# Performance work log

Measured on AMD Instinct MI355X. Metric: run time of the kernel, lower is better.

The kernel has to match this reference:

```python
import jax, jax.numpy as jnp
from jax import lax
import numpy as np

B = 256
# conv stack: (in_ch, out_ch, kernel)
_CONV_CFG = [(1, 3, 4), (3, 9, 4), (9, 12, 4), (12, 15, 4), (15, 15, 3)]
_FLAT = 15 * 4 ** 4  # 3840, matches nn.Linear(15*(18-14)**4, 100)


def _conv4d(x, w, b):
    """True 4D valid convolution. x: [B,C,d1,d2,d3,d4], w: [O,I,k,k,k,k]."""
    dn = lax.conv_dimension_numbers(x.shape, w.shape, ('NCDHWX', 'OIDHWX', 'NCDHWX'))
    y = lax.conv_general_dilated(x, w, window_strides=(1, 1, 1, 1),
                                 padding='VALID', dimension_numbers=dn)
    return y + b.reshape((1, -1) + (1,) * 4)


def setup_inputs() -> dict:
    key = jax.random.key(0)
    ks = jax.random.split(key, 16)
    inp = {'x': jax.random.normal(ks[0], (B, 1, 18, 18, 18, 18), dtype=jnp.float32)}
    for i, (ci, co, k) in enumerate(_CONV_CFG, start=1):
        fan_in = ci * k ** 4
        inp[f'w{i}'] = jax.random.normal(ks[2 * i - 1], (co, ci, k, k, k, k), dtype=jnp.float32) / np.sqrt(fan_in)
        inp[f'b{i}'] = jnp.zeros((co,), dtype=jnp.float32)
    inp['fc1_w'] = jax.random.normal(ks[11], (_FLAT, 100), dtype=jnp.float32) / np.sqrt(_FLAT)
    inp['fc1_b'] = jnp.zeros((100,), dtype=jnp.float32)
    inp['fc2_w'] = jax.random.normal(ks[12], (100, 1), dtype=jnp.float32) / np.sqrt(100.0)
    inp['fc2_b'] = jnp.zeros((1,), dtype=jnp.float32)
    return inp


def reference(x, w1, b1, w2, b2, w3, b3, w4, b4, w5, b5, fc1_w, fc1_b, fc2_w, fc2_b):
    h = jax.nn.relu(_conv4d(x, w1, b1))
    h = jax.nn.relu(_conv4d(h, w2, b2))
    h = jax.nn.relu(_conv4d(h, w3, b3))
    h = jax.nn.relu(_conv4d(h, w4, b4))
    h = jax.nn.relu(_conv4d(h, w5, b5))  # [B,15,4,4,4,4]
    h = h.reshape(h.shape[0], -1)        # [B,3840], torch Flatten order
    # Dropout(0.5) is identity at inference (eval mode)
    h = jax.nn.relu(h @ fc1_w + fc1_b)
    return jax.nn.sigmoid(h @ fc2_w + fc2_b)  # [B,1]
```

## Files before the change

kernel.cpp:

```cpp
#include <hip/hip_runtime.h>
#include <hip/hip_bf16.h>


#define BATCH 256
typedef unsigned int u32;
typedef float    f32x4  __attribute__((ext_vector_type(4)));
typedef float    f32x16 __attribute__((ext_vector_type(16)));
typedef _Float16 f16x8  __attribute__((ext_vector_type(8)));

struct __attribute__((packed, aligned(4))) f16x8w { f16x8 v; };

__global__ void cvt_f32_f16(const float* __restrict__ in, _Float16* __restrict__ o, int n8) {
    int i = blockIdx.x * blockDim.x + threadIdx.x;
    if (i >= n8) return;
    const f32x4* p = (const f32x4*)(in + (size_t)i * 8);
    f32x4 a = p[0], b = p[1];
    f16x8 v;
    #pragma unroll
    for (int j = 0; j < 4; ++j) { v[j] = (_Float16)a[j]; v[4 + j] = (_Float16)b[j]; }
    *(f16x8*)(o + (size_t)i * 8) = v;
}

template<int COUT, int CIN, int KS, int S>
__global__ void prepack_v5(const float* __restrict__ w, _Float16* __restrict__ wf) {
    constexpr int STEPS = CIN * KS * 2 * KS;
    constexpr int TOT = STEPS * 512;
    int idx = blockIdx.x * 256 + threadIdx.x;
    if (idx >= TOT) return;
    int j    = idx & 7;
    int lane = (idx >> 3) & 63;
    int st   = idx >> 9;
    int k1 = st % KS;
    int r1 = st / KS;
    int k3p = r1 & 1;
    int r2  = r1 >> 1;
    int k2 = r2 % KS;
    int ci = r2 / KS;
    int gg = lane >> 5, col = lane & 31;
    int oc = col / S, s = col % S;
    int k3 = k3p * 2 + gg;
    int k4 = j - s;
    float v = 0.0f;
    if (oc < COUT && k3 < KS && k4 >= 0 && k4 < KS)
        v = w[((((oc * CIN + ci) * KS + k1) * KS + k2) * KS + k3) * KS + k4];
    wf[idx] = (_Float16)v;
}

template<int BYTES>
__device__ __forceinline__ void stage_b(const _Float16* gsrc, char* ldst, int tid) {
    constexpr int N16 = BYTES / 16;
    const int wv = tid >> 6, ln = tid & 63;
    #pragma unroll
    for (int it = 0; it * 256 < N16; ++it) {
        int u16 = it * 256 + (wv << 6);
        if (u16 < N16) {
            const char* gp = (const char*)gsrc + (size_t)(u16 + ln) * 16;
            __builtin_amdgcn_global_load_lds(
                (const __attribute__((address_space(1))) unsigned int*)gp,
                (__attribute__((address_space(3))) unsigned int*)(ldst + u16 * 16),
                16, 0, 0);
        }
    }
}

template<int CIN, int COUT, int KS, int DIN, int DP, int S, int OP, int T,
         int CG, int MINW>
__launch_bounds__(256, MINW)
__global__ void conv4d_v10(const _Float16* __restrict__ x,
                           const _Float16* __restrict__ wf,
                           const float* __restrict__ bias,
                           _Float16* __restrict__ out) {
    constexpr int DOUT = DIN - KS + 1;
    constexpr int NB   = (DOUT + S - 1) / S;
    constexpr int PCOL = DOUT * DOUT * NB;
    constexpr int NTC  = (PCOL + 31) / 32;
    constexpr int NG   = DOUT / T;
    static_assert(DOUT % T == 0, "T must divide DOUT");
    constexpr int XD2 = DIN * DP;
    constexpr int XD1 = DIN * XD2;
    constexpr int XCI = DIN * XD1;
    constexpr int GROUPS = CIN * KS * 2;
    static_assert(GROUPS % CG == 0, "CG must divide GROUPS");
    constexpr int CSTEPS = CG * KS;
    constexpr int CBYTES = CSTEPS * 1024;
    constexpr int NCHUNK = GROUPS / CG;
    constexpr int NBUF   = (NCHUNK > 1) ? 2 : 1;
    constexpr int AJ = T + KS - 1;
    constexpr int W  = T + 1;
    constexpr u32 NW   = (u32)BATCH * NG * NTC;
    constexpr u32 POUT = (u32)DOUT * DOUT * DOUT * OP;

    __shared__ char bsm[NBUF * CBYTES];
    const int tid = threadIdx.x;
    u32 wid = blockIdx.x * 4u + (u32)(tid >> 6);
    if (wid >= NW) wid = NW - 1u;
    const int ln = tid & 63;
    const int g  = ln >> 5;
    const int r  = ln & 31;

    u32 tc = wid % (u32)NTC;  u32 q = wid / (u32)NTC;
    u32 d1g = q % (u32)NG;    u32 b = q / (u32)NG;
    u32 rr = tc * 32u + (u32)r;  if (rr >= (u32)PCOL) rr = (u32)PCOL - 1u;
    u32 u  = rr % (u32)NB;    u32 q2 = rr / (u32)NB;
    u32 d3 = q2 % (u32)DOUT;  u32 d2 = q2 / (u32)DOUT;

    const u32 lanebase2 = (b * (u32)(CIN * XCI) + d1g * (u32)(T * XD1)
                         + d2 * (u32)XD2 + d3 * (u32)DP + (u32)(g * DP)
                         + u * (u32)S) * 2u;
    const char* xc = (const char*)x;

    f32x16 acc[T];
    #pragma unroll
    for (int t = 0; t < T; ++t)
        #pragma unroll
        for (int i = 0; i < 16; ++i) acc[t][i] = 0.0f;

    stage_b<CBYTES>(wf, &bsm[0], tid);

    #pragma unroll 1
    for (int ch = 0; ch < NCHUNK; ++ch) {
        __syncthreads();
        if (NCHUNK > 1 && ch + 1 < NCHUNK)
            stage_b<CBYTES>(wf + (size_t)(ch + 1) * CSTEPS * 512,
                            &bsm[((ch + 1) & 1) * CBYTES], tid);
        const char* bb = &bsm[(ch & 1) * (NBUF > 1 ? CBYTES : 0)] + ln * 16;
        #pragma unroll
        for (int gi = 0; gi < CG; ++gi) {
            int grp = ch * CG + gi;
            int k3p = grp & 1;
            int k2  = (grp >> 1) % KS;
            int ci  = (grp >> 1) / KS;
            u32 goff = ((u32)ci * (u32)XCI + (u32)k2 * (u32)XD2
                      + (u32)(k3p * 2 * DP)) * 2u;
            const char* ap = xc + lanebase2 + goff;

            f16x8 ar[W];
            #pragma unroll
            for (int j = 0; j < T; ++j)
                ar[j] = ((const f16x8w*)(ap + j * (XD1 * 2)))->v;
            #pragma unroll
            for (int k1 = 0; k1 < KS; ++k1) {
                if (T + k1 < AJ)
                    ar[(T + k1) % W] = ((const f16x8w*)(ap + (T + k1) * (XD1 * 2)))->v;
                f16x8 bf = *(const f16x8*)(bb + (gi * KS + k1) * 1024);
                #pragma unroll
                for (int t = 0; t < T; ++t)
                    acc[t] = __builtin_amdgcn_mfma_f32_32x32x16_f16(
                        ar[(k1 + t) % W], bf, acc[t], 0, 0, 0);
            }
        }
    }

    const int oc = r / S, s = r % S;
    if (oc >= COUT) return;
    float bv = bias[oc];
    #pragma unroll
    for (int reg = 0; reg < 16; ++reg) {
        int rowoff = (reg & 3) + 8 * (reg >> 2) + 4 * g;
        u32 rr2 = tc * 32u + (u32)rowoff;
        if (rr2 >= (u32)PCOL) rr2 = (u32)PCOL - 1u;
        u32 uu = rr2 % (u32)NB;  u32 qq = rr2 / (u32)NB;
        u32 dd3 = qq % (u32)DOUT; u32 dd2 = qq / (u32)DOUT;
        u32 d4 = uu * (u32)S + (u32)s;
        if (d4 < (u32)DOUT) {
            u32 obase = (b * (u32)COUT + (u32)oc) * POUT
                      + (dd2 * (u32)DOUT + dd3) * (u32)OP + d4
                      + d1g * (u32)(T * DOUT * DOUT * OP);
            #pragma unroll
            for (int t = 0; t < T; ++t)
                out[obase + (u32)t * (u32)(DOUT * DOUT * OP)]
                    = (_Float16)fmaxf(acc[t][reg] + bv, 0.0f);
        }
    }
}

__global__ void prepack_fc1(const float* __restrict__ w, _Float16* __restrict__ wf) {
    int idx = blockIdx.x * 256 + threadIdx.x;
    if (idx >= 430080) return;
    int j    = idx & 7;
    int lane = (idx >> 3) & 63;
    int t9   = idx >> 9;
    int st   = t9 % 120;
    int ni   = t9 / 120;
    int k    = st * 32 + (lane >> 4) * 8 + j;
    int col  = ni * 16 + (lane & 15);
    wf[idx] = (_Float16)((col < 100) ? w[k * 100 + col] : 0.0f);
}

__launch_bounds__(256)
__global__ void fc1_mfma(const _Float16* __restrict__ h,
                         const _Float16* __restrict__ wfc,
                         const float* __restrict__ bias,
                         float* __restrict__ o) {
    int wv   = blockIdx.x * 4 + (threadIdx.x >> 6);
    int lane = threadIdx.x & 63;
    int r = lane & 15, g = lane >> 4;
    int mi = wv / 7, ni = wv % 7;
    const f16x8* A  = (const f16x8*)(h + (size_t)(mi * 16 + r) * 3840);
    const f16x8* Bv = (const f16x8*)wfc;
    f32x4 acc = {0.f, 0.f, 0.f, 0.f};
    #pragma unroll 4
    for (int st = 0; st < 120; ++st) {
        f16x8 a = A[st * 4 + g];
        f16x8 b = Bv[(ni * 120 + st) * 64 + lane];
        acc = __builtin_amdgcn_mfma_f32_16x16x32_f16(a, b, acc, 0, 0, 0);
    }
    int col = ni * 16 + r;
    if (col < 100) {
        float bv = bias[col];
        #pragma unroll
        for (int i = 0; i < 4; ++i) {
            int row = mi * 16 + g * 4 + i;
            o[row * 100 + col] = fmaxf(acc[i] + bv, 0.0f);
        }
    }
}

__global__ void fc2_sigmoid(const float* __restrict__ h,
                            const float* __restrict__ w,
                            const float* __restrict__ bias,
                            float* __restrict__ out) {
    int b = blockIdx.x * blockDim.x + threadIdx.x;
    if (b >= BATCH) return;
    const float* hb = h + b * 100;
    float acc = bias[0];
    #pragma unroll
    for (int j = 0; j < 100; ++j)
        acc = fmaf(hb[j], w[j], acc);
    out[b] = 1.0f / (1.0f + expf(-acc));
}

extern "C" void kernel_launch(void* const* d_in, const int* in_sizes, int n_in,
                              void* d_out, int out_size, void* d_ws, size_t ws_size,
                              hipStream_t stream) {
    const float* x    = (const float*)d_in[0];
    const float* w1   = (const float*)d_in[1];
    const float* b1   = (const float*)d_in[2];
    const float* w2   = (const float*)d_in[3];
    const float* b2   = (const float*)d_in[4];
    const float* w3   = (const float*)d_in[5];
    const float* b3   = (const float*)d_in[6];
    const float* w4   = (const float*)d_in[7];
    const float* b4   = (const float*)d_in[8];
    const float* w5   = (const float*)d_in[9];
    const float* b5   = (const float*)d_in[10];
    const float* fc1w = (const float*)d_in[11];
    const float* fc1b = (const float*)d_in[12];
    const float* fc2w = (const float*)d_in[13];
    const float* fc2b = (const float*)d_in[14];
    float* out = (float*)d_out;

    _Float16* W = (_Float16*)d_ws;
    size_t cur = 0;
    auto alloc = [&](size_t n) { _Float16* p = W + cur; cur += (n + 255) & ~(size_t)255; return p; };
    _Float16* x16 = alloc(26873856);
    _Float16* h1  = alloc(41472000);
    _Float16* h2  = alloc(47775744);
    _Float16* h3  = alloc(22394880);
    _Float16* h4  = alloc(4976640);
    _Float16* h5  = alloc(983040);
    _Float16* wf1 = alloc(16384);
    _Float16* wf2 = alloc(49152);
    _Float16* wf3 = alloc(147456);
    _Float16* wf4 = alloc(196608);
    _Float16* wf5 = alloc(138240);
    _Float16* wfc = alloc(430080);
    float* fc1out = (float*)alloc(51200 + 256);

    cvt_f32_f16<<<13122, 256, 0, stream>>>(x, x16, 3359232);

    prepack_v5<3, 1, 4, 4><<<64,  256, 0, stream>>>(w1, wf1);
    prepack_v5<9, 3, 4, 2><<<192, 256, 0, stream>>>(w2, wf2);
    prepack_v5<12, 9, 4, 2><<<576, 256, 0, stream>>>(w3, wf3);
    prepack_v5<15, 12, 4, 2><<<768, 256, 0, stream>>>(w4, wf4);
    prepack_v5<15, 15, 3, 2><<<540, 256, 0, stream>>>(w5, wf5);
    prepack_fc1<<<1680, 256, 0, stream>>>(fc1w, wfc);

    conv4d_v10<1, 3, 4, 18, 18, 4, 16, 3, 8, 4><<<9280, 256, 0, stream>>>(x16, wf1, b1, h1);
    conv4d_v10<3, 9, 4, 15, 16, 2, 12, 6, 4, 3><<<3456, 256, 0, stream>>>(h1, wf2, b2, h2);
    conv4d_v10<9, 12, 4, 12, 12, 2, 10, 3, 4, 4><<<2496, 256, 0, stream>>>(h2, wf3, b3, h3);
    conv4d_v10<12, 15, 4, 9, 10, 2, 6, 3, 4, 4><<<512, 256, 0, stream>>>(h3, wf4, b4, h4);
    conv4d_v10<15, 15, 3, 6, 6, 2, 4, 4, 6, 4><<<64, 256, 0, stream>>>(h4, wf5, b5, h5);

    fc1_mfma<<<28, 256, 0, stream>>>(h5, wfc, fc1b, fc1out);
    fc2_sigmoid<<<1, 256, 0, stream>>>(fc1out, fc2w, fc2b, out);
}
```

Baseline: 931.3 us.

## Write shifted copy of conv1 output so conv2 uses stride-3 column packing

Conv1 now also writes a copy of its output shifted by one element. Conv2 reads from this copy whenever its base offset is odd, so its 16-byte A-fragment loads stay aligned even with a stride S of 3. Conv2 moves from stride 2 to stride 3 packing, which reduces its column tiles and launch size (2304 blocks instead of 3456). Its weights are prepacked for S=3 and workspace buffers are reused to fit the extra copy. The cost is roughly double the store traffic for conv1's large output.

```diff
diff --git a/kernel.cpp b/kernel.cpp
--- a/kernel.cpp
+++ b/kernel.cpp
@@ -64,12 +64,14 @@
 }
 
 template<int CIN, int COUT, int KS, int DIN, int DP, int S, int OP, int T,
-         int CG, int MINW>
+         int CG, int MINW, int SODD, int WSHIFT>
 __launch_bounds__(256, MINW)
-__global__ void conv4d_v10(const _Float16* __restrict__ x,
+__global__ void conv4d_v13(const _Float16* __restrict__ x,
+                           const _Float16* __restrict__ xs,
                            const _Float16* __restrict__ wf,
                            const float* __restrict__ bias,
-                           _Float16* __restrict__ out) {
+                           _Float16* __restrict__ out,
+                           _Float16* __restrict__ outs) {
     constexpr int DOUT = DIN - KS + 1;
     constexpr int NB   = (DOUT + S - 1) / S;
     constexpr int PCOL = DOUT * DOUT * NB;
@@ -104,10 +106,16 @@
     u32 u  = rr % (u32)NB;    u32 q2 = rr / (u32)NB;
     u32 d3 = q2 % (u32)DOUT;  u32 d2 = q2 / (u32)DOUT;
 
-    const u32 lanebase2 = (b * (u32)(CIN * XCI) + d1g * (u32)(T * XD1)
-                         + d2 * (u32)XD2 + d3 * (u32)DP + (u32)(g * DP)
-                         + u * (u32)S) * 2u;
-    const char* xc = (const char*)x;
+    const u32 o = b * (u32)(CIN * XCI) + d1g * (u32)(T * XD1)
+                + d2 * (u32)XD2 + d3 * (u32)DP + (u32)(g * DP) + u * (u32)S;
+    const char* xb;
+    if (SODD) {
+        u32 p = o & 1u;
+        xb = p ? ((const char*)xs + (size_t)(o - 1u) * 2)
+               : ((const char*)x  + (size_t)o * 2);
+    } else {
+        xb = (const char*)x + (size_t)o * 2;
+    }
 
     f32x16 acc[T];
     #pragma unroll
@@ -132,7 +140,7 @@
             int ci  = (grp >> 1) / KS;
             u32 goff = ((u32)ci * (u32)XCI + (u32)k2 * (u32)XD2
                       + (u32)(k3p * 2 * DP)) * 2u;
-            const char* ap = xc + lanebase2 + goff;
+            const char* ap = xb + goff;
 
             f16x8 ar[W];
             #pragma unroll
@@ -167,9 +175,12 @@
                       + (dd2 * (u32)DOUT + dd3) * (u32)OP + d4
                       + d1g * (u32)(T * DOUT * DOUT * OP);
             #pragma unroll
-            for (int t = 0; t < T; ++t)
-                out[obase + (u32)t * (u32)(DOUT * DOUT * OP)]
-                    = (_Float16)fmaxf(acc[t][reg] + bv, 0.0f);
+            for (int t = 0; t < T; ++t) {
+                u32 oidx = obase + (u32)t * (u32)(DOUT * DOUT * OP);
+                _Float16 v = (_Float16)fmaxf(acc[t][reg] + bv, 0.0f);
+                out[oidx] = v;
+                if (WSHIFT) { if (oidx >= 1u) outs[oidx - 1u] = v; }
+            }
         }
     }
 }
@@ -251,36 +262,40 @@
     float* out = (float*)d_out;
 
     _Float16* W = (_Float16*)d_ws;
-    size_t cur = 0;
-    auto alloc = [&](size_t n) { _Float16* p = W + cur; cur += (n + 255) & ~(size_t)255; return p; };
-    _Float16* x16 = alloc(26873856);
-    _Float16* h1  = alloc(41472000);
-    _Float16* h2  = alloc(47775744);
-    _Float16* h3  = alloc(22394880);
-    _Float16* h4  = alloc(4976640);
-    _Float16* h5  = alloc(983040);
-    _Float16* wf1 = alloc(16384);
-    _Float16* wf2 = alloc(49152);
-    _Float16* wf3 = alloc(147456);
-    _Float16* wf4 = alloc(196608);
-    _Float16* wf5 = alloc(138240);
-    _Float16* wfc = alloc(430080);
-    float* fc1out = (float*)alloc(51200 + 256);
+    _Float16* x16 = W;
+    _Float16* h1  = W + 26873856;
+    _Float16* h1s = W + 68345856;
+    _Float16* h2  = W + 109817856;
+    _Float16* wf1 = W + 157593600;
+    _Float16* wf2 = W + 157609984;
+    _Float16* wf3 = W + 157659136;
+    _Float16* wf4 = W + 157806592;
+    _Float16* wf5 = W + 158003200;
+    _Float16* wfc = W + 158141440;
+    float* fc1out = (float*)(W + 158571520);
+    _Float16* h3  = h1s;
+    _Float16* h4  = h1s + 22394880;
+    _Float16* h5  = h1s + 27371520;
 
     cvt_f32_f16<<<13122, 256, 0, stream>>>(x, x16, 3359232);
 
     prepack_v5<3, 1, 4, 4><<<64,  256, 0, stream>>>(w1, wf1);
-    prepack_v5<9, 3, 4, 2><<<192, 256, 0, stream>>>(w2, wf2);
+    prepack_v5<9, 3, 4, 3><<<192, 256, 0, stream>>>(w2, wf2);
     prepack_v5<12, 9, 4, 2><<<576, 256, 0, stream>>>(w3, wf3);
     prepack_v5<15, 12, 4, 2><<<768, 256, 0, stream>>>(w4, wf4);
     prepack_v5<15, 15, 3, 2><<<540, 256, 0, stream>>>(w5, wf5);
     prepack_fc1<<<1680, 256, 0, stream>>>(fc1w, wfc);
 
-    conv4d_v10<1, 3, 4, 18, 18, 4, 16, 3, 8, 4><<<9280, 256, 0, stream>>>(x16, wf1, b1, h1);
-    conv4d_v10<3, 9, 4, 15, 16, 2, 12, 6, 4, 3><<<3456, 256, 0, stream>>>(h1, wf2, b2, h2);
-    conv4d_v10<9, 12, 4, 12, 12, 2, 10, 3, 4, 4><<<2496, 256, 0, stream>>>(h2, wf3, b3, h3);
-    conv4d_v10<12, 15, 4, 9, 10, 2, 6, 3, 4, 4><<<512, 256, 0, stream>>>(h3, wf4, b4, h4);
-    conv4d_v10<15, 15, 3, 6, 6, 2, 4, 4, 6, 4><<<64, 256, 0, stream>>>(h4, wf5, b5, h5);
+    conv4d_v13<1, 3, 4, 18, 18, 4, 16, 3, 8, 4, 0, 1>
+        <<<9280, 256, 0, stream>>>(x16, x16, wf1, b1, h1, h1s);
+    conv4d_v13<3, 9, 4, 15, 16, 3, 12, 6, 4, 3, 1, 0>
+        <<<2304, 256, 0, stream>>>(h1, h1s, wf2, b2, h2, h2);
+    conv4d_v13<9, 12, 4, 12, 12, 2, 10, 3, 4, 4, 0, 0>
+        <<<2496, 256, 0, stream>>>(h2, h2, wf3, b3, h3, h3);
+    conv4d_v13<12, 15, 4, 9, 10, 2, 6, 3, 4, 4, 0, 0>
+        <<<512, 256, 0, stream>>>(h3, h3, wf4, b4, h4, h4);
+    conv4d_v13<15, 15, 3, 6, 6, 2, 4, 4, 6, 4, 0, 0>
+        <<<64, 256, 0, stream>>>(h4, h4, wf5, b5, h5, h5);
 
     fc1_mfma<<<28, 256, 0, stream>>>(h5, wfc, fc1b, fc1out);
     fc2_sigmoid<<<1, 256, 0, stream>>>(fc1out, fc2w, fc2b, out);
```

Result: faster. 905.9 us (-2.7%).
